# Kernel optimization log

Measured on AMD Instinct MI355X. Metric: run time of the kernel, lower is better.

Reference implementation:

```python
import jax, jax.numpy as jnp
import numpy as np

NUM_EMBEDDINGS = 8192
EMBEDDING_DIM = 256
BETA = 0.25


def setup_inputs() -> dict:
    key = jax.random.key(0)
    k1, k2 = jax.random.split(key)
    z = jax.random.normal(k1, (16, 256, 32, 32), dtype=jnp.float32)
    # torch init: uniform(-1/K, 1/K)
    emb_w = jax.random.uniform(k2, (NUM_EMBEDDINGS, EMBEDDING_DIM),
                               dtype=jnp.float32,
                               minval=-1.0 / NUM_EMBEDDINGS,
                               maxval=1.0 / NUM_EMBEDDINGS)
    return {"z": z, "emb_w": emb_w}


def reference(z, emb_w):
    B, C, H, W = z.shape
    z_bhwc = jnp.transpose(z, (0, 2, 3, 1))          # [B,H,W,C]
    flat = z_bhwc.reshape(-1, C)                      # [N,C]
    d = (jnp.sum(flat * flat, axis=1, keepdims=True)
         + jnp.sum(emb_w * emb_w, axis=1)
         - 2.0 * flat @ emb_w.T)                      # [N,K]
    idx = jnp.argmin(d, axis=1)                       # [N]
    # direct gather (mathematically identical to one-hot @ emb_w)
    quantized = emb_w[idx].reshape(z_bhwc.shape)      # [B,H,W,C]
    q_latent_loss = jnp.mean((jax.lax.stop_gradient(quantized) - z_bhwc) ** 2)
    e_latent_loss = jnp.mean((quantized - jax.lax.stop_gradient(z_bhwc)) ** 2)
    loss = q_latent_loss + BETA * e_latent_loss
    # straight-through estimator
    quantized_st = z_bhwc + jax.lax.stop_gradient(quantized - z_bhwc)
    out = jnp.transpose(quantized_st, (0, 3, 1, 2))   # [B,C,H,W]
    return out, loss, idx.reshape(B, -1)
```

## Files before the change

### kernel.cpp

```cpp
#include <hip/hip_runtime.h>
#include <cstdint>
#include <cstddef>

#define N_PIX   16384
#define K_EMB   8192
#define DDIM    256

#define WS_A8       0
#define WS_E8       4194304
#define WS_KEYS     6291456
#define WS_ZSQ      23068672
#define WS_ESQ      23134208
#define WS_LOSS     23166976
#define WS_CNT      23166984

typedef float f32x16 __attribute__((ext_vector_type(16)));
typedef int   i32x4  __attribute__((ext_vector_type(4)));
typedef int   i32x8  __attribute__((ext_vector_type(8)));

__device__ __forceinline__ unsigned int f32_sortable(float f) {
    unsigned int u = __float_as_uint(f);
    return (u & 0x80000000u) ? ~u : (u | 0x80000000u);
}

__device__ __forceinline__ unsigned char f2fp8(float x) {
    unsigned ub = __float_as_uint(x);
    unsigned sgn = (ub >> 24) & 0x80u;
    unsigned b = ub & 0x7FFFFFFFu;
    unsigned out;
    if (__uint_as_float(b) < 0.015625f) {
        out = (unsigned)(int)rintf(__uint_as_float(b) * 512.0f);
    } else {
        unsigned r = b + 0x7FFFFu + ((b >> 20) & 1u);
        int er = (int)(r >> 23) - 127;
        out = (unsigned)(((er + 7) << 3) | ((r >> 20) & 7u));
    }
    return (unsigned char)(out | sgn);
}

#if defined(__has_builtin)
#if __has_builtin(__builtin_amdgcn_cvt_pk_fp8_f32)
#define HAVE_CVT_FP8 1
#endif
#if __has_builtin(__builtin_amdgcn_fmed3f)
#define HAVE_FMED3 1
#endif
#endif

__device__ __forceinline__ unsigned pack4_fp8(float a, float b, float c, float d) {
#ifdef HAVE_CVT_FP8
    int pk = 0;
    pk = __builtin_amdgcn_cvt_pk_fp8_f32(a, b, pk, false);
    pk = __builtin_amdgcn_cvt_pk_fp8_f32(c, d, pk, true);
    return (unsigned)pk;
#else
    return (unsigned)f2fp8(a) | ((unsigned)f2fp8(b) << 8)
         | ((unsigned)f2fp8(c) << 16) | ((unsigned)f2fp8(d) << 24);
#endif
}

__device__ __forceinline__ void async16(const unsigned char* g, unsigned char* l) {
    __builtin_amdgcn_global_load_lds(
        (const __attribute__((address_space(1))) void*)g,
        (__attribute__((address_space(3))) void*)l, 16, 0, 0);
}

__global__ __launch_bounds__(256) void prep_kernel(
        const float* __restrict__ z, const float* __restrict__ emb,
        unsigned char* __restrict__ Af8, unsigned char* __restrict__ Ef8,
        float* __restrict__ zsq, float* __restrict__ esq,
        double* __restrict__ lossAcc, unsigned* __restrict__ doneCnt) {
    __shared__ float tile[32][257];
    __shared__ float sqs[32][17];
    int blk = blockIdx.x;
    int t   = threadIdx.x;
    if (blk < 512) {
        int b   = blk >> 5;
        int hw0 = (blk & 31) * 32;
        const float* zb = z + (size_t)b * 262144 + hw0;
        int c0  = t >> 3;
        int px4 = t & 7;
#pragma unroll
        for (int cc = 0; cc < 8; ++cc) {
            int c = cc * 32 + c0;
            float4 v = *(const float4*)&zb[(size_t)c * 1024 + px4 * 4];
            tile[px4 * 4 + 0][c] = v.x;
            tile[px4 * 4 + 1][c] = v.y;
            tile[px4 * 4 + 2][c] = v.z;
            tile[px4 * 4 + 3][c] = v.w;
        }
        __syncthreads();
        int p0 = b * 1024 + hw0;
        int wv = t >> 6, lane = t & 63;
#pragma unroll
        for (int iter = 0; iter < 8; ++iter) {
            int pl = iter * 4 + wv;
            unsigned pk = pack4_fp8(tile[pl][lane * 4 + 0], tile[pl][lane * 4 + 1],
                                    tile[pl][lane * 4 + 2], tile[pl][lane * 4 + 3]);
            int p  = p0 + pl;
            int mbb = p >> 7, r = p & 127;
            int c = lane * 4;
            *(unsigned*)(Af8 + (size_t)mbb * 32768
                         + (c >> 6) * 8192 + r * 64 + (c & 63)) = pk;
        }
        {
            int row = t >> 3, s0 = t & 7;
            const float* rp = tile[row];
            float a0 = 0.f, a1 = 0.f;
#pragma unroll
            for (int i = 0; i < 16; ++i) {
                float x0 = rp[s0 + 8 * i];
                a0 = __fadd_rn(a0, __fmul_rn(x0, x0));
            }
#pragma unroll
            for (int i = 0; i < 16; ++i) {
                float x1 = rp[128 + s0 + 8 * i];
                a1 = __fadd_rn(a1, __fmul_rn(x1, x1));
            }
            sqs[row][s0]     = a0;
            sqs[row][s0 + 8] = a1;
        }
        __syncthreads();
        if (t < 32) {
            const float* r = sqs[t];
            float h0 = __fadd_rn(
                __fadd_rn(__fadd_rn(r[0], r[1]), __fadd_rn(r[2], r[3])),
                __fadd_rn(__fadd_rn(r[4], r[5]), __fadd_rn(r[6], r[7])));
            float h1 = __fadd_rn(
                __fadd_rn(__fadd_rn(r[8], r[9]), __fadd_rn(r[10], r[11])),
                __fadd_rn(__fadd_rn(r[12], r[13]), __fadd_rn(r[14], r[15])));
            zsq[p0 + t] = __fadd_rn(h0, h1);
        }
        if (blk == 0 && t == 0) { *lossAcc = 0.0; *doneCnt = 0u; }
    } else {
        int k0 = (blk - 512) * 32;
        const float4* eg = (const float4*)(emb + (size_t)k0 * DDIM);
#pragma unroll
        for (int i = 0; i < 8; ++i) {
            int idx = i * 256 + t;
            int row = idx >> 6, c4 = idx & 63;
            float4 v = eg[idx];
            *(float4*)&tile[row][c4 * 4] = v;
        }
        __syncthreads();
#pragma unroll
        for (int i = 0; i < 8; ++i) {
            int idx = i * 256 + t;
            int row = idx >> 6, c4 = idx & 63;
            const float* rp = &tile[row][c4 * 4];
            int kg = k0 + row;
            int nbb = kg >> 7, rr = kg & 127;
            int c  = c4 * 4;
            int kk = c >> 6, kl = c & 63;
            int s  = kl >> 4;
            int pos = kk * 8192 + rr * 64
                    + ((s ^ ((rr >> 1) & 3)) << 4) + (kl & 15);
            *(unsigned*)(Ef8 + (size_t)nbb * 32768 + pos) =
                pack4_fp8(rp[0] * 8192.0f, rp[1] * 8192.0f,
                          rp[2] * 8192.0f, rp[3] * 8192.0f);
        }
        {
            int row = t >> 3, s0 = t & 7;
            const float* rp = tile[row];
            float a0 = 0.f, a1 = 0.f;
#pragma unroll
            for (int i = 0; i < 16; ++i) {
                float x0 = rp[s0 + 8 * i];
                a0 = __fadd_rn(a0, __fmul_rn(x0, x0));
            }
#pragma unroll
            for (int i = 0; i < 16; ++i) {
                float x1 = rp[128 + s0 + 8 * i];
                a1 = __fadd_rn(a1, __fmul_rn(x1, x1));
            }
            sqs[row][s0]     = a0;
            sqs[row][s0 + 8] = a1;
        }
        __syncthreads();
        if (t < 32) {
            const float* r = sqs[t];
            float h0 = __fadd_rn(
                __fadd_rn(__fadd_rn(r[0], r[1]), __fadd_rn(r[2], r[3])),
                __fadd_rn(__fadd_rn(r[4], r[5]), __fadd_rn(r[6], r[7])));
            float h1 = __fadd_rn(
                __fadd_rn(__fadd_rn(r[8], r[9]), __fadd_rn(r[10], r[11])),
                __fadd_rn(__fadd_rn(r[12], r[13]), __fadd_rn(r[14], r[15])));
            esq[k0 + t] = __fadd_rn(h0, h1);
        }
    }
}

__device__ __forceinline__ unsigned pack_key(float w) {
    float uf = __builtin_fmaf(w, -512.0f, 262144.0f);
    uf = fminf(uf, 524287.0f);
    unsigned u = (unsigned)uf;
    return (u << 13) | (__float_as_uint(w) & 0x1FFFu);
}

__global__ __launch_bounds__(256) void mfma_score_kernel(
        const unsigned char* __restrict__ Af8,
        const unsigned char* __restrict__ Ef8,
        unsigned int* __restrict__ keys) {
    union __align__(16) SM {
        unsigned char Bs[2][32768];
        struct { uint2 ep[128][33]; } e;
    };
    __shared__ SM sm;

    const int g  = blockIdx.x;
    const int mb = blockIdx.y;
    const int t = threadIdx.x;
    const int w = t >> 6, lane = t & 63;
    const int l31 = lane & 31, h = lane >> 5;

    {
        const unsigned char* Eg = Ef8 + (size_t)(g * 4) * 32768 + t * 16;
#pragma unroll
        for (int ch = 0; ch < 8; ++ch)
            async16(Eg + ch * 4096, &sm.Bs[0][ch * 4096 + t * 16]);
    }

    i32x8 afr[4];
    {
        const unsigned char* Ab = Af8 + (size_t)mb * 32768;
        int r = w * 32 + l31;
#pragma unroll
        for (int kk = 0; kk < 4; ++kk) {
            const unsigned char* p = Ab + kk * 8192 + r * 64 + h * 32;
            i32x4 lo = *(const i32x4*)p;
            i32x4 hi = *(const i32x4*)(p + 16);
            afr[kk] = __builtin_shufflevector(lo, hi, 0, 1, 2, 3, 4, 5, 6, 7);
        }
    }

    const float NEGINF = __int_as_float(0xFF800000);
    float t2a[16], t2b[16];
#pragma unroll
    for (int q = 0; q < 16; ++q) { t2a[q] = NEGINF; t2b[q] = NEGINF; }

    __syncthreads();

#pragma unroll 1
    for (int j = 0; j < 4; ++j) {
        const int cur = j & 1, nxt = cur ^ 1;

        if (j < 3) {
            const unsigned char* Eg =
                Ef8 + (size_t)(g * 4 + j + 1) * 32768 + t * 16;
#pragma unroll
            for (int ch = 0; ch < 8; ++ch)
                async16(Eg + ch * 4096, &sm.Bs[nxt][ch * 4096 + t * 16]);
        }

        const int nb = g * 4 + j;
#pragma unroll
        for (int ct = 0; ct < 4; ++ct) {
            f32x16 acc;
#pragma unroll
            for (int q = 0; q < 16; ++q) acc[q] = 0.f;

            const int c  = ct * 32 + l31;
            const int m  = (c >> 1) & 3;
            const int s0 = h * 2;
            __builtin_amdgcn_s_setprio(1);
#pragma unroll
            for (int kk = 0; kk < 4; ++kk) {
                int base = kk * 8192 + c * 64;
                i32x4 lo = *(const i32x4*)
                    &sm.Bs[cur][base + ((s0 ^ m) << 4)];
                i32x4 hi = *(const i32x4*)
                    &sm.Bs[cur][base + (((s0 + 1) ^ m) << 4)];
                i32x8 bf = __builtin_shufflevector(lo, hi,
                                                   0, 1, 2, 3, 4, 5, 6, 7);
                acc = __builtin_amdgcn_mfma_scale_f32_32x32x64_f8f6f4(
                        afr[kk], bf, acc,
                        0, 0,
                        0, 0x7F7F7F7F,
                        0, 0x7F7F7F7F);
            }
            __builtin_amdgcn_s_setprio(0);

            const unsigned idxc = (unsigned)(nb * 128 + c);
#pragma unroll
            for (int q = 0; q < 16; ++q) {
                float v = acc[q];
                float wv = __uint_as_float(
                    (__float_as_uint(v) & 0xFFFFE000u) | idxc);
                float a0 = t2a[q], b0 = t2b[q];
#ifdef HAVE_FMED3
                float bn = __builtin_amdgcn_fmed3f(a0, wv, b0);
                t2a[q] = fmaxf(a0, wv);
                t2b[q] = bn;
#else
                float mn = fminf(a0, wv);
                t2a[q] = fmaxf(a0, wv);
                t2b[q] = fmaxf(b0, mn);
#endif
            }
        }
        __syncthreads();
    }

#pragma unroll
    for (int q = 0; q < 16; ++q) {
        int row = w * 32 + (q & 3) + 8 * (q >> 2) + 4 * h;
        sm.e.ep[row][l31] = make_uint2(pack_key(t2a[q]), pack_key(t2b[q]));
    }
    __syncthreads();

    {
        int row = t >> 1, half = t & 1, h0 = half * 16;
        uint2 mv = sm.e.ep[row][h0];
#pragma unroll
        for (int i = 1; i < 16; ++i) {
            uint2 av = sm.e.ep[row][h0 + i];
            unsigned n0 = min(mv.x, av.x);
            unsigned n1 = min(max(mv.x, av.x), min(mv.y, av.y));
            mv.x = n0; mv.y = n1;
        }
        ((uint2*)keys)[(size_t)(g * 2 + half) * N_PIX + (mb * 128 + row)] = mv;
    }
}

__global__ __launch_bounds__(256) void final_kernel(
        const unsigned int* __restrict__ keys,
        const float* __restrict__ z, const float* __restrict__ emb,
        const float* __restrict__ zsq, const float* __restrict__ esq,
        float* __restrict__ out, float* __restrict__ idx_out,
        float* __restrict__ loss_out,
        double* __restrict__ lossAcc, unsigned* __restrict__ doneCnt) {
    __shared__ float ztile[32][257];
    __shared__ uint2 kt[32][33];
    __shared__ unsigned short scand[32][64];
    __shared__ unsigned long long ckey[2048];
    __shared__ int   soff[33];
    __shared__ int   scnt[32];
    __shared__ unsigned char pxmap[2048];
    __shared__ float szs[32];
    __shared__ int   sidx[32];

    int blk = blockIdx.x;
    int b = blk >> 5, hh2 = blk & 31;
    int t = threadIdx.x;
    int p0 = b * 1024 + hh2 * 32;
    const float* zb = z + (size_t)b * 262144 + hh2 * 32;
    {
        int c0 = t >> 3, px4 = t & 7;
#pragma unroll
        for (int cc = 0; cc < 8; ++cc) {
            int c = cc * 32 + c0;
            float4 v = *(const float4*)&zb[(size_t)c * 1024 + px4 * 4];
            ztile[px4 * 4 + 0][c] = v.x;
            ztile[px4 * 4 + 1][c] = v.y;
            ztile[px4 * 4 + 2][c] = v.z;
            ztile[px4 * 4 + 3][c] = v.w;
        }
    }
    {
        const uint2* kg = (const uint2*)keys;
#pragma unroll
        for (int itr = 0; itr < 4; ++itr) {
            int idx = itr * 256 + t;
            int px = idx & 31, hf = idx >> 5;
            kt[px][hf] = kg[(size_t)hf * N_PIX + p0 + px];
        }
    }
    if (t < 32) szs[t] = zsq[p0 + t];
    __syncthreads();

    {
        int wq = t >> 6, lane = t & 63;
#pragma unroll 1
        for (int i = 0; i < 8; ++i) {
            int px = wq * 8 + i;
            uint2 ka = (lane < 32) ? kt[px][lane] : make_uint2(~0u, ~0u);
            unsigned m = min(ka.x, ka.y);
#pragma unroll
            for (int off = 32; off >= 1; off >>= 1)
                m = min(m, (unsigned)__shfl_xor((int)m, off, 64));
            unsigned thr = (m >> 13) + 1600;

            bool h0 = (lane < 32) && ((ka.x >> 13) <= thr);
            bool h1 = (lane < 32) && ((ka.y >> 13) <= thr);
            unsigned long long m0 = __ballot(h0);
            unsigned long long m1 = __ballot(h1);
            int c0 = __popcll(m0);
            unsigned long long below = (lane == 63) ? ~0ull >> 1
                                     : ((1ull << lane) - 1);
            if (h0) scand[px][__popcll(m0 & below)] =
                (unsigned short)(ka.x & 0x1FFFu);
            if (h1) scand[px][c0 + __popcll(m1 & below)] =
                (unsigned short)(ka.y & 0x1FFFu);
            if (lane == 0) scnt[px] = c0 + __popcll(m1);
        }
    }
    __syncthreads();

    if (t < 64) {
        int v = (t < 32) ? scnt[t] : 0;
#pragma unroll
        for (int o = 1; o < 32; o <<= 1) {
            int u = __shfl_up(v, o, 64);
            if (t >= o) v += u;
        }
        if (t < 32) soff[t + 1] = v;
        if (t == 0) soff[0] = 0;
    }
    __syncthreads();
    int total = soff[32];
    for (int f = t; f < total; f += 256) {
        int lo = 0, hi = 31;
        while (lo < hi) {
            int mid = (lo + hi + 1) >> 1;
            if (soff[mid] <= f) lo = mid; else hi = mid - 1;
        }
        pxmap[f] = (unsigned char)lo;
    }
    __syncthreads();

    {
        int gid = t >> 4, l16 = t & 15;
        const float4* emb4 = (const float4*)emb;
#pragma unroll 1
        for (int f = gid; f < total; f += 16) {
            int px = pxmap[f];
            int k  = scand[px][f - soff[px]];
            double d = 0.0;
#pragma unroll
            for (int q = 0; q < 4; ++q) {
                float4 ev = emb4[(size_t)k * 64 + q * 16 + l16];
                const float* zp = &ztile[px][(q * 16 + l16) * 4];
                d += (double)zp[0] * ev.x + (double)zp[1] * ev.y
                   + (double)zp[2] * ev.z + (double)zp[3] * ev.w;
            }
#pragma unroll
            for (int o = 1; o < 16; o <<= 1) d += __shfl_xor(d, o, 64);
            if (l16 == 0) {
                float df = (float)d;
                float s  = __fsub_rn(__fadd_rn(szs[px], esq[k]),
                                     __fmul_rn(2.0f, df));
                ckey[f] = ((unsigned long long)f32_sortable(s) << 32)
                        | (unsigned)k;
            }
        }
    }
    __syncthreads();

    {
        int ci = t & 15;
#pragma unroll
        for (int pass = 0; pass < 2; ++pass) {
            int cpx = (t >> 4) + pass * 16;
            unsigned long long best = ~0ull;
            for (int f = soff[cpx] + ci; f < soff[cpx + 1]; f += 16) {
                unsigned long long v = ckey[f];
                best = v < best ? v : best;
            }
#pragma unroll
            for (int o = 1; o < 16; o <<= 1) {
                unsigned long long ov =
                    (unsigned long long)__shfl_xor((long long)best, o, 64);
                best = ov < best ? ov : best;
            }
            if (ci == 0) {
                int k = (int)(unsigned)(best & 0xffffffffu);
                sidx[cpx] = k;
                idx_out[p0 + cpx] = (float)k;
            }
        }
    }
    __syncthreads();

    int px2 = t & 31, cy = t >> 5;
    int kk = sidx[px2];
    const float* er = emb + (size_t)kk * DDIM;
    float* ob = out + (size_t)b * 262144 + hh2 * 32;
    float local = 0.f;
#pragma unroll 4
    for (int it = 0; it < 32; ++it) {
        int c = it * 8 + cy;
        float q = er[c];
        float d = q - ztile[px2][c];
        ob[(size_t)c * 1024 + px2] = q;
        local += d * d;
    }
#pragma unroll
    for (int off = 32; off >= 1; off >>= 1) local += __shfl_down(local, off, 64);
    __shared__ float wsum[4];
    if ((t & 63) == 0) wsum[t >> 6] = local;
    __syncthreads();
    if (t == 0) {
        double s = (double)wsum[0] + (double)wsum[1]
                 + (double)wsum[2] + (double)wsum[3];
        atomicAdd(lossAcc, s);
        __threadfence();
        unsigned old = atomicAdd(doneCnt, 1u);
        if (old == 511u) {
            double tot = atomicAdd(lossAcc, 0.0);
            *loss_out = (float)(tot * (1.25 / 4194304.0));
        }
    }
}

extern "C" void kernel_launch(void* const* d_in, const int* in_sizes, int n_in,
                              void* d_out, int out_size, void* d_ws, size_t ws_size,
                              hipStream_t stream) {
    const float* z   = (const float*)d_in[0];
    const float* emb = (const float*)d_in[1];
    float* out = (float*)d_out;
    char* ws = (char*)d_ws;

    unsigned char* Af8 = (unsigned char*)(ws + WS_A8);
    unsigned char* Ef8 = (unsigned char*)(ws + WS_E8);
    unsigned int* keys = (unsigned int*)(ws + WS_KEYS);
    float* zsq      = (float*)(ws + WS_ZSQ);
    float* esq      = (float*)(ws + WS_ESQ);
    double* lossAcc = (double*)(ws + WS_LOSS);
    unsigned* doneCnt = (unsigned*)(ws + WS_CNT);

    prep_kernel<<<768, 256, 0, stream>>>(z, emb, Af8, Ef8, zsq, esq,
                                         lossAcc, doneCnt);
    mfma_score_kernel<<<dim3(16, 128), 256, 0, stream>>>(Af8, Ef8, keys);
    final_kernel<<<512, 256, 0, stream>>>(keys, z, emb, zsq, esq,
                                          out, out + 4194305, out + 4194304,
                                          lossAcc, doneCnt);
}
```

Measured before the change: 164.2 us.

## Restructure z prep and split output write into coalesced separate kernel

The z half of prep_kernel now runs 128 blocks that each handle 128 pixels in 32-channel chunks. It writes 16-byte FP8 stores and keeps per-pixel partial squared norms in shared memory, instead of using 512 blocks with 4-byte stores. The gather, output write and loss accumulation move out of final_kernel into a new write_kernel. That kernel transposes gathered embedding rows through shared memory so the NCHW output is written with coalesced float4 stores. This adds a fourth kernel launch, re-reads z and the indices from global memory, and uses fewer blocks, which may reduce parallelism. An unused np_pairwise_sq256 helper is also added.

```diff
diff --git a/kernel.cpp b/kernel.cpp
--- a/kernel.cpp
+++ b/kernel.cpp
@@ -65,89 +65,114 @@
         (__attribute__((address_space(3))) void*)l, 16, 0, 0);
 }
 
+__device__ __forceinline__ float np_pairwise_sq256(const float* row) {
+    float r[16];
+#pragma unroll
+    for (int j = 0; j < 16; ++j) r[j] = 0.f;
+#pragma unroll
+    for (int c = 0; c < 256; ++c) {
+        float x  = row[c];
+        float sq = __fmul_rn(x, x);
+        int slot = ((c >> 7) << 3) | (c & 7);
+        r[slot] = __fadd_rn(r[slot], sq);
+    }
+    float h0 = __fadd_rn(
+        __fadd_rn(__fadd_rn(r[0], r[1]), __fadd_rn(r[2], r[3])),
+        __fadd_rn(__fadd_rn(r[4], r[5]), __fadd_rn(r[6], r[7])));
+    float h1 = __fadd_rn(
+        __fadd_rn(__fadd_rn(r[8], r[9]), __fadd_rn(r[10], r[11])),
+        __fadd_rn(__fadd_rn(r[12], r[13]), __fadd_rn(r[14], r[15])));
+    return __fadd_rn(h0, h1);
+}
+
 __global__ __launch_bounds__(256) void prep_kernel(
         const float* __restrict__ z, const float* __restrict__ emb,
         unsigned char* __restrict__ Af8, unsigned char* __restrict__ Ef8,
         float* __restrict__ zsq, float* __restrict__ esq,
         double* __restrict__ lossAcc, unsigned* __restrict__ doneCnt) {
-    __shared__ float tile[32][257];
-    __shared__ float sqs[32][17];
+    union SH {
+        struct { float tz[32][132]; float sacc[128][17]; } zp;
+        struct { float tile[32][257]; float sqs[32][17]; } ep;
+    };
+    __shared__ SH sh;
     int blk = blockIdx.x;
     int t   = threadIdx.x;
-    if (blk < 512) {
-        int b   = blk >> 5;
-        int hw0 = (blk & 31) * 32;
-        const float* zb = z + (size_t)b * 262144 + hw0;
-        int c0  = t >> 3;
-        int px4 = t & 7;
-#pragma unroll
-        for (int cc = 0; cc < 8; ++cc) {
-            int c = cc * 32 + c0;
-            float4 v = *(const float4*)&zb[(size_t)c * 1024 + px4 * 4];
-            tile[px4 * 4 + 0][c] = v.x;
-            tile[px4 * 4 + 1][c] = v.y;
-            tile[px4 * 4 + 2][c] = v.z;
-            tile[px4 * 4 + 3][c] = v.w;
+    if (blk < 128) {
+        int b = blk >> 3, mbl = blk & 7;
+        const float* zb = z + (size_t)b * 262144 + mbl * 128;
+        for (int i = t; i < 128 * 17; i += 256)
+            ((float*)sh.zp.sacc)[i] = 0.f;
+#pragma unroll 1
+        for (int ch = 0; ch < 8; ++ch) {
+            int c0 = ch * 32;
+            __syncthreads();
+#pragma unroll
+            for (int s = 0; s < 4; ++s) {
+                int u = t + 256 * s;
+                int row = u >> 5, col4 = u & 31;
+                float4 v = *(const float4*)&zb[(size_t)(c0 + row) * 1024
+                                               + col4 * 4];
+                *(float4*)&sh.zp.tz[row][col4 * 4] = v;
+            }
+            __syncthreads();
+            {
+                int r = t >> 1, cb = (t & 1) * 16;
+                uint4 val;
+                val.x = pack4_fp8(sh.zp.tz[cb + 0][r],  sh.zp.tz[cb + 1][r],
+                                  sh.zp.tz[cb + 2][r],  sh.zp.tz[cb + 3][r]);
+                val.y = pack4_fp8(sh.zp.tz[cb + 4][r],  sh.zp.tz[cb + 5][r],
+                                  sh.zp.tz[cb + 6][r],  sh.zp.tz[cb + 7][r]);
+                val.z = pack4_fp8(sh.zp.tz[cb + 8][r],  sh.zp.tz[cb + 9][r],
+                                  sh.zp.tz[cb + 10][r], sh.zp.tz[cb + 11][r]);
+                val.w = pack4_fp8(sh.zp.tz[cb + 12][r], sh.zp.tz[cb + 13][r],
+                                  sh.zp.tz[cb + 14][r], sh.zp.tz[cb + 15][r]);
+                *(uint4*)(Af8 + (size_t)blk * 32768 + (c0 >> 6) * 8192
+                          + r * 64 + (c0 & 32) + (t & 1) * 16) = val;
+            }
+            {
+                int r  = t >> 1;
+                int sb = (c0 >= 128) ? 8 : 0;
+#pragma unroll
+                for (int q = 0; q < 4; ++q) {
+                    int j0 = (t & 1) * 4 + q;
+                    float v = sh.zp.sacc[r][sb + j0];
+#pragma unroll
+                    for (int m = 0; m < 4; ++m) {
+                        float x = sh.zp.tz[j0 + 8 * m][r];
+                        v = __fadd_rn(v, __fmul_rn(x, x));
+                    }
+                    sh.zp.sacc[r][sb + j0] = v;
+                }
+            }
         }
         __syncthreads();
-        int p0 = b * 1024 + hw0;
-        int wv = t >> 6, lane = t & 63;
-#pragma unroll
-        for (int iter = 0; iter < 8; ++iter) {
-            int pl = iter * 4 + wv;
-            unsigned pk = pack4_fp8(tile[pl][lane * 4 + 0], tile[pl][lane * 4 + 1],
-                                    tile[pl][lane * 4 + 2], tile[pl][lane * 4 + 3]);
-            int p  = p0 + pl;
-            int mbb = p >> 7, r = p & 127;
-            int c = lane * 4;
-            *(unsigned*)(Af8 + (size_t)mbb * 32768
-                         + (c >> 6) * 8192 + r * 64 + (c & 63)) = pk;
-        }
-        {
-            int row = t >> 3, s0 = t & 7;
-            const float* rp = tile[row];
-            float a0 = 0.f, a1 = 0.f;
-#pragma unroll
-            for (int i = 0; i < 16; ++i) {
-                float x0 = rp[s0 + 8 * i];
-                a0 = __fadd_rn(a0, __fmul_rn(x0, x0));
-            }
-#pragma unroll
-            for (int i = 0; i < 16; ++i) {
-                float x1 = rp[128 + s0 + 8 * i];
-                a1 = __fadd_rn(a1, __fmul_rn(x1, x1));
-            }
-            sqs[row][s0]     = a0;
-            sqs[row][s0 + 8] = a1;
-        }
-        __syncthreads();
-        if (t < 32) {
-            const float* r = sqs[t];
+        if (t < 128) {
+            const float* r = sh.zp.sacc[t];
             float h0 = __fadd_rn(
                 __fadd_rn(__fadd_rn(r[0], r[1]), __fadd_rn(r[2], r[3])),
                 __fadd_rn(__fadd_rn(r[4], r[5]), __fadd_rn(r[6], r[7])));
             float h1 = __fadd_rn(
                 __fadd_rn(__fadd_rn(r[8], r[9]), __fadd_rn(r[10], r[11])),
                 __fadd_rn(__fadd_rn(r[12], r[13]), __fadd_rn(r[14], r[15])));
-            zsq[p0 + t] = __fadd_rn(h0, h1);
+            zsq[(size_t)b * 1024 + mbl * 128 + t] = __fadd_rn(h0, h1);
         }
         if (blk == 0 && t == 0) { *lossAcc = 0.0; *doneCnt = 0u; }
     } else {
-        int k0 = (blk - 512) * 32;
+        int k0 = (blk - 128) * 32;
         const float4* eg = (const float4*)(emb + (size_t)k0 * DDIM);
 #pragma unroll
         for (int i = 0; i < 8; ++i) {
             int idx = i * 256 + t;
             int row = idx >> 6, c4 = idx & 63;
             float4 v = eg[idx];
-            *(float4*)&tile[row][c4 * 4] = v;
+            *(float4*)&sh.ep.tile[row][c4 * 4] = v;
         }
         __syncthreads();
 #pragma unroll
         for (int i = 0; i < 8; ++i) {
             int idx = i * 256 + t;
             int row = idx >> 6, c4 = idx & 63;
-            const float* rp = &tile[row][c4 * 4];
+            const float* rp = &sh.ep.tile[row][c4 * 4];
             int kg = k0 + row;
             int nbb = kg >> 7, rr = kg & 127;
             int c  = c4 * 4;
@@ -161,7 +186,7 @@
         }
         {
             int row = t >> 3, s0 = t & 7;
-            const float* rp = tile[row];
+            const float* rp = sh.ep.tile[row];
             float a0 = 0.f, a1 = 0.f;
 #pragma unroll
             for (int i = 0; i < 16; ++i) {
@@ -173,12 +198,12 @@
                 float x1 = rp[128 + s0 + 8 * i];
                 a1 = __fadd_rn(a1, __fmul_rn(x1, x1));
             }
-            sqs[row][s0]     = a0;
-            sqs[row][s0 + 8] = a1;
+            sh.ep.sqs[row][s0]     = a0;
+            sh.ep.sqs[row][s0 + 8] = a1;
         }
         __syncthreads();
         if (t < 32) {
-            const float* r = sqs[t];
+            const float* r = sh.ep.sqs[t];
             float h0 = __fadd_rn(
                 __fadd_rn(__fadd_rn(r[0], r[1]), __fadd_rn(r[2], r[3])),
                 __fadd_rn(__fadd_rn(r[4], r[5]), __fadd_rn(r[6], r[7])));
@@ -326,9 +351,7 @@
         const unsigned int* __restrict__ keys,
         const float* __restrict__ z, const float* __restrict__ emb,
         const float* __restrict__ zsq, const float* __restrict__ esq,
-        float* __restrict__ out, float* __restrict__ idx_out,
-        float* __restrict__ loss_out,
-        double* __restrict__ lossAcc, unsigned* __restrict__ doneCnt) {
+        float* __restrict__ idx_out) {
     __shared__ float ztile[32][257];
     __shared__ uint2 kt[32][33];
     __shared__ unsigned short scand[32][64];
@@ -337,7 +360,6 @@
     __shared__ int   scnt[32];
     __shared__ unsigned char pxmap[2048];
     __shared__ float szs[32];
-    __shared__ int   sidx[32];
 
     int blk = blockIdx.x;
     int b = blk >> 5, hh2 = blk & 31;
@@ -462,31 +484,66 @@
                     (unsigned long long)__shfl_xor((long long)best, o, 64);
                 best = ov < best ? ov : best;
             }
-            if (ci == 0) {
-                int k = (int)(unsigned)(best & 0xffffffffu);
-                sidx[cpx] = k;
-                idx_out[p0 + cpx] = (float)k;
-            }
-        }
-    }
-    __syncthreads();
-
-    int px2 = t & 31, cy = t >> 5;
-    int kk = sidx[px2];
-    const float* er = emb + (size_t)kk * DDIM;
-    float* ob = out + (size_t)b * 262144 + hh2 * 32;
+            if (ci == 0)
+                idx_out[p0 + cpx] = (float)(int)(unsigned)(best & 0xffffffffu);
+        }
+    }
+}
+
+__global__ __launch_bounds__(256) void write_kernel(
+        const float* __restrict__ z, const float* __restrict__ emb,
+        const float* __restrict__ idx_in, float* __restrict__ out,
+        float* __restrict__ loss_out,
+        double* __restrict__ lossAcc, unsigned* __restrict__ doneCnt) {
+    __shared__ float etile[32][132];
+    __shared__ int   kidx[128];
+    __shared__ float wsum[4];
+    int blk = blockIdx.x;
+    int b = blk >> 3, mbl = blk & 7;
+    int t = threadIdx.x;
+    size_t pbase = (size_t)b * 1024 + mbl * 128;
+    if (t < 128) kidx[t] = (int)idx_in[pbase + t];
+    const float* zb = z + (size_t)b * 262144 + mbl * 128;
+    float* ob = out + (size_t)b * 262144 + mbl * 128;
     float local = 0.f;
-#pragma unroll 4
-    for (int it = 0; it < 32; ++it) {
-        int c = it * 8 + cy;
-        float q = er[c];
-        float d = q - ztile[px2][c];
-        ob[(size_t)c * 1024 + px2] = q;
-        local += d * d;
-    }
-#pragma unroll
-    for (int off = 32; off >= 1; off >>= 1) local += __shfl_down(local, off, 64);
-    __shared__ float wsum[4];
+    __syncthreads();
+#pragma unroll 1
+    for (int ch = 0; ch < 8; ++ch) {
+        int c0 = ch * 32;
+        if (ch) __syncthreads();
+        {
+            int px = t >> 1, part = t & 1;
+            int k = kidx[px];
+            const float4* er = (const float4*)(emb + (size_t)k * 256 + c0);
+#pragma unroll
+            for (int i = 0; i < 4; ++i) {
+                float4 v = er[part * 4 + i];
+                int cr = part * 16 + i * 4;
+                etile[cr + 0][px] = v.x;
+                etile[cr + 1][px] = v.y;
+                etile[cr + 2][px] = v.z;
+                etile[cr + 3][px] = v.w;
+            }
+        }
+        __syncthreads();
+        {
+            int row = t >> 3;
+            int pxb = (t & 7) * 16;
+#pragma unroll
+            for (int s2 = 0; s2 < 4; ++s2) {
+                int px = pxb + s2 * 4;
+                float4 zv = *(const float4*)&zb[(size_t)(c0 + row) * 1024 + px];
+                float4 ev = *(const float4*)&etile[row][px];
+                *(float4*)&ob[(size_t)(c0 + row) * 1024 + px] = ev;
+                float d0 = ev.x - zv.x, d1 = ev.y - zv.y;
+                float d2 = ev.z - zv.z, d3 = ev.w - zv.w;
+                local += d0 * d0 + d1 * d1 + d2 * d2 + d3 * d3;
+            }
+        }
+    }
+#pragma unroll
+    for (int off = 32; off >= 1; off >>= 1)
+        local += __shfl_down(local, off, 64);
     if ((t & 63) == 0) wsum[t >> 6] = local;
     __syncthreads();
     if (t == 0) {
@@ -495,7 +552,7 @@
         atomicAdd(lossAcc, s);
         __threadfence();
         unsigned old = atomicAdd(doneCnt, 1u);
-        if (old == 511u) {
+        if (old == 127u) {
             double tot = atomicAdd(lossAcc, 0.0);
             *loss_out = (float)(tot * (1.25 / 4194304.0));
         }
@@ -518,10 +575,11 @@
     double* lossAcc = (double*)(ws + WS_LOSS);
     unsigned* doneCnt = (unsigned*)(ws + WS_CNT);
 
-    prep_kernel<<<768, 256, 0, stream>>>(z, emb, Af8, Ef8, zsq, esq,
+    prep_kernel<<<384, 256, 0, stream>>>(z, emb, Af8, Ef8, zsq, esq,
                                          lossAcc, doneCnt);
     mfma_score_kernel<<<dim3(16, 128), 256, 0, stream>>>(Af8, Ef8, keys);
     final_kernel<<<512, 256, 0, stream>>>(keys, z, emb, zsq, esq,
-                                          out, out + 4194305, out + 4194304,
-                                          lossAcc, doneCnt);
-}
+                                          out + 4194305);
+    write_kernel<<<128, 256, 0, stream>>>(z, emb, out + 4194305, out,
+                                          out + 4194304, lossAcc, doneCnt);
+}
```

After: 168.4 us. 1.03x slower.
